# Kernel optimization log

Hardware: AMD Instinct MI355X
Metric: run time of the kernel (lower is better)

The kernel has to match this reference:

```python
import jax, jax.numpy as jnp
import numpy as np

D_MODEL, N_HEADS, RANK = 1024, 16, 32
HEAD_DIM = D_MODEL // N_HEADS
B, S = 4, 2048


def setup_inputs() -> dict:
    key = jax.random.key(0)
    ks = jax.random.split(key, 8)
    inp = {
        "x": jax.random.normal(ks[0], (B, S, D_MODEL), dtype=jnp.float32),
        "mask": jnp.ones((B, S), dtype=jnp.int32),
        "qkv_u": jax.random.normal(ks[1], (D_MODEL, RANK), jnp.float32) / D_MODEL ** 0.5,
        "qkv_v": jax.random.normal(ks[2], (RANK, 3 * D_MODEL), jnp.float32) / RANK ** 0.5,
        "qkv_b": jnp.zeros((3 * D_MODEL,), jnp.float32),
        "u_attn": jax.random.normal(ks[3], (N_HEADS, HEAD_DIM, RANK), jnp.float32) / HEAD_DIM ** 0.5,
        "v_attn": jax.random.normal(ks[4], (N_HEADS, RANK, HEAD_DIM), jnp.float32) / RANK ** 0.5,
        "out_u": jax.random.normal(ks[5], (D_MODEL, RANK), jnp.float32) / D_MODEL ** 0.5,
        "out_v": jax.random.normal(ks[6], (RANK, D_MODEL), jnp.float32) / RANK ** 0.5,
        "out_b": jnp.zeros((D_MODEL,), jnp.float32),
    }
    return inp


def reference(x, mask, qkv_u, qkv_v, qkv_b, u_attn, v_attn, out_u, out_v, out_b):
    bs, seq_len, d_model = x.shape
    n_heads, head_dim, rank = u_attn.shape
    scale = 1.0 / jnp.sqrt(jnp.float32(rank))

    # Low-rank QKV projection: [B,S,3D]
    qkv = (x @ qkv_u) @ qkv_v + qkv_b
    q, k, v = jnp.split(qkv, 3, axis=-1)

    def to_heads(t):  # [B,S,D] -> [B,H,S,hd]
        return t.reshape(bs, seq_len, n_heads, head_dim).transpose(0, 2, 1, 3)

    q, k, v = to_heads(q), to_heads(k), to_heads(v)

    # Rank-projected Q/K: [B,H,S,r]
    q_low = jnp.einsum("bhsd,hdr->bhsr", q, u_attn)
    k_low = jnp.einsum("bhtd,hdr->bhtr", k, u_attn)
    scores = jnp.einsum("bhsr,bhtr->bhst", q_low, k_low) * scale

    # mask: [B,S] keys; masked_fill where mask == 0
    scores = jnp.where(mask[:, None, None, :] == 0, jnp.float32(-jnp.inf), scores)
    attn = jax.nn.softmax(scores, axis=-1)  # dropout is identity in eval

    v_low = jnp.einsum("bhtd,hdr->bhtr", v, u_attn)
    context_low = jnp.einsum("bhst,bhtr->bhsr", attn, v_low)
    context = jnp.einsum("bhsr,hrd->bhsd", context_low, v_attn)
    context = context.transpose(0, 2, 1, 3).reshape(bs, seq_len, d_model)

    return (context @ out_u) @ out_v + out_b
```

## Files before the change

### kernel.cpp

```cpp
#include <hip/hip_runtime.h>
#include <hip/hip_bf16.h>

typedef unsigned int u32;
typedef unsigned short u16;
typedef __attribute__((ext_vector_type(8))) __bf16 bf16x8;
typedef __attribute__((ext_vector_type(16))) float f32x16;
typedef __attribute__((ext_vector_type(2))) unsigned int u32x2;

#define QSCALE 0.25505418f
#define MFMA __builtin_amdgcn_mfma_f32_32x32x16_bf16

static __device__ __forceinline__ u16 f2b(float f) {
  __hip_bfloat16 h = __float2bfloat16(f);
  return *reinterpret_cast<u16*>(&h);
}
static __device__ __forceinline__ u32 cvtpk(float lo, float hi) {
  u32 r;
  asm("v_cvt_pk_bf16_f32 %0, %1, %2" : "=v"(r) : "v"(lo), "v"(hi));
  return r;
}

static __device__ __forceinline__ float xhalf_sum(float v) {
#if __has_builtin(__builtin_amdgcn_permlane32_swap)
  u32 a = __float_as_uint(v);
  u32x2 r = __builtin_amdgcn_permlane32_swap(a, a, false, false);
  return __uint_as_float(r[0]) + __uint_as_float(r[1]);
#else
  return v + __shfl_xor(v, 32);
#endif
}

static __device__ __forceinline__ int tau(int p) {
  int g = p >> 2;
  int gk = (g & 4) | ((g & 1) << 1) | ((g >> 1) & 1);
  return (gk << 2) | (p & 3);
}

__global__ __launch_bounds__(256) void k_prep(const float* __restrict__ qkv_v,
                                              const float* __restrict__ qkv_b,
                                              const float* __restrict__ u_attn,
                                              const float* __restrict__ v_attn,
                                              const float* __restrict__ out_u,
                                              const float* __restrict__ qkv_u,
                                              const float* __restrict__ out_v,
                                              u16* __restrict__ WQT, u16* __restrict__ WKT,
                                              u16* __restrict__ WVT, float* __restrict__ BQKV,
                                              u16* __restrict__ WOT, u16* __restrict__ UT,
                                              u16* __restrict__ OVT) {
  int blk = blockIdx.x;
  int tid = threadIdx.x;
  if (blk < 16) {
    int h = blk;
    int r = tid & 31, g = tid >> 5;
    for (int rp = g; rp < 32; rp += 8) {
      float aq = 0.f, ak = 0.f, av = 0.f;
      for (int d = 0; d < 64; ++d) {
        float u = u_attn[(h * 64 + d) * 32 + r];
        aq += qkv_v[rp * 3072 + h * 64 + d] * u;
        ak += qkv_v[rp * 3072 + 1024 + h * 64 + d] * u;
        av += qkv_v[rp * 3072 + 2048 + h * 64 + d] * u;
      }
      WQT[(h * 32 + r) * 32 + rp] = f2b(aq);
      WKT[(h * 32 + r) * 32 + rp] = f2b(ak);
      WVT[(h * 32 + r) * 32 + rp] = f2b(av);
    }
    for (int rr = g; rr < 32; rr += 8) {
      float a = 0.f;
      for (int d = 0; d < 64; ++d)
        a += v_attn[(h * 32 + rr) * 64 + d] * out_u[(h * 64 + d) * 32 + r];
      WOT[r * 512 + h * 32 + rr] = f2b(a);
    }
    if (tid < 32) {
      float aq = 0.f, ak = 0.f, av = 0.f;
      for (int d = 0; d < 64; ++d) {
        float u = u_attn[(h * 64 + d) * 32 + r];
        aq += qkv_b[h * 64 + d] * u;
        ak += qkv_b[1024 + h * 64 + d] * u;
        av += qkv_b[2048 + h * 64 + d] * u;
      }
      BQKV[h * 32 + r] = aq;
      BQKV[512 + h * 32 + r] = ak;
      BQKV[1024 + h * 32 + r] = av;
    }
  } else if (blk < 24) {
    int kb = (blk - 16) * 128;
    for (int i = tid; i < 4096; i += 256) {
      int r = i >> 7, kl = i & 127;
      UT[r * 1024 + kb + kl] = f2b(qkv_u[(kb + kl) * 32 + r]);
    }
  } else {
    int db = (blk - 24) * 128;
    for (int i = tid; i < 4096; i += 256) {
      int dl = i >> 5, r = i & 31;
      OVT[(db + dl) * 32 + r] = f2b(out_v[r * 1024 + db + dl]);
    }
  }
}

__global__ __launch_bounds__(256) void k_proj(const float* __restrict__ x,
                                              const u16* __restrict__ UT,
                                              u16* __restrict__ T) {
  __shared__ float red[4][32][33];
  int tid = threadIdx.x;
  int w = tid >> 6, l = tid & 63, lo = l & 31, hi = l >> 5;
  int m0 = blockIdx.x * 32;
  const float* xp = x + (size_t)(m0 + lo) * 1024 + w * 256 + hi * 8;
  const u16* up = UT + lo * 1024 + w * 256 + hi * 8;
  f32x16 acc = {};
  for (int s = 0; s < 16; ++s) {
    float4 x0 = *(const float4*)(xp);
    float4 x1 = *(const float4*)(xp + 4);
    xp += 16;
    union { bf16x8 v; u32 u[4]; } af;
    af.u[0] = cvtpk(x0.x, x0.y);
    af.u[1] = cvtpk(x0.z, x0.w);
    af.u[2] = cvtpk(x1.x, x1.y);
    af.u[3] = cvtpk(x1.z, x1.w);
    bf16x8 bf = *(const bf16x8*)(up);
    up += 16;
    acc = MFMA(af.v, bf, acc, 0, 0, 0);
  }
#pragma unroll
  for (int i = 0; i < 16; ++i)
    red[w][(i & 3) + 8 * (i >> 2) + 4 * hi][lo] = acc[i];
  __syncthreads();
  int m = tid >> 3, c = (tid & 7) * 4;
  float v0 = red[0][m][c + 0] + red[1][m][c + 0] + red[2][m][c + 0] + red[3][m][c + 0];
  float v1 = red[0][m][c + 1] + red[1][m][c + 1] + red[2][m][c + 1] + red[3][m][c + 1];
  float v2 = red[0][m][c + 2] + red[1][m][c + 2] + red[2][m][c + 2] + red[3][m][c + 2];
  float v3 = red[0][m][c + 3] + red[1][m][c + 3] + red[2][m][c + 3] + red[3][m][c + 3];
  uint2 o;
  o.x = cvtpk(v0, v1);
  o.y = cvtpk(v2, v3);
  *(uint2*)(T + (size_t)(m0 + m) * 32 + c) = o;
}

__global__ __launch_bounds__(256) void k_lowproj(const u16* __restrict__ T,
                                                 const u16* __restrict__ WQT,
                                                 const u16* __restrict__ WKT,
                                                 const u16* __restrict__ WVT,
                                                 const float* __restrict__ BQKV,
                                                 u16* __restrict__ QL, u16* __restrict__ KF,
                                                 u16* __restrict__ VF) {
  __shared__ float vtf[32][132];
  int tid = threadIdx.x;
  int w = tid >> 6, l = tid & 63, lo = l & 31, hi = l >> 5;
  int blk = blockIdx.x;
  int bh = blk >> 4, sb = (blk & 15) * 128;
  int b = bh >> 4, h = bh & 15;
  int s0 = sb + w * 32;

  const u16* wq = WQT + (h * 32 + lo) * 32 + hi * 8;
  const u16* wk = WKT + (h * 32 + lo) * 32 + hi * 8;
  const u16* wv = WVT + (h * 32 + lo) * 32 + hi * 8;
  bf16x8 aq0 = *(const bf16x8*)(wq), aq1 = *(const bf16x8*)(wq + 16);
  bf16x8 ak0 = *(const bf16x8*)(wk), ak1 = *(const bf16x8*)(wk + 16);
  bf16x8 av0 = *(const bf16x8*)(wv), av1 = *(const bf16x8*)(wv + 16);

  const u16* tp = T + (size_t)(b * 2048 + s0 + lo) * 32 + hi * 8;
  bf16x8 tb0 = *(const bf16x8*)(tp), tb1 = *(const bf16x8*)(tp + 16);

  f32x16 cq = {}, ck = {}, cv = {};
  cq = MFMA(aq0, tb0, cq, 0, 0, 0);
  cq = MFMA(aq1, tb1, cq, 0, 0, 0);
  ck = MFMA(ak0, tb0, ck, 0, 0, 0);
  ck = MFMA(ak1, tb1, ck, 0, 0, 0);
  cv = MFMA(av0, tb0, cv, 0, 0, 0);
  cv = MFMA(av1, tb1, cv, 0, 0, 0);

  size_t sg = (size_t)bh * 2048 + s0 + lo;
  size_t tbase = (size_t)bh * 65536 + (size_t)((sb >> 5) + w) * 1024;
  int slp = w * 32 + tau(lo);
#pragma unroll
  for (int g2 = 0; g2 < 4; ++g2) {
    float4 bq4 = *(const float4*)(BQKV + h * 32 + g2 * 8 + 4 * hi);
    float4 bk4 = *(const float4*)(BQKV + 512 + h * 32 + g2 * 8 + 4 * hi);
    float4 bv4 = *(const float4*)(BQKV + 1024 + h * 32 + g2 * 8 + 4 * hi);
    float q0 = (cq[4 * g2 + 0] + bq4.x) * QSCALE;
    float q1 = (cq[4 * g2 + 1] + bq4.y) * QSCALE;
    float q2 = (cq[4 * g2 + 2] + bq4.z) * QSCALE;
    float q3 = (cq[4 * g2 + 3] + bq4.w) * QSCALE;
    uint2 qo; qo.x = cvtpk(q0, q1); qo.y = cvtpk(q2, q3);
    *(uint2*)(QL + sg * 32 + g2 * 8 + 4 * hi) = qo;
    uint2 ko;
    ko.x = cvtpk(ck[4 * g2 + 0] + bk4.x, ck[4 * g2 + 1] + bk4.y);
    ko.y = cvtpk(ck[4 * g2 + 2] + bk4.z, ck[4 * g2 + 3] + bk4.w);
    *(uint2*)(KF + tbase + (g2 >> 1) * 512 + (g2 & 1) * 256 + lo * 8 + 4 * hi) = ko;
    int rbase = g2 * 8 + 4 * hi;
    vtf[rbase + 0][slp] = cv[4 * g2 + 0] + bv4.x;
    vtf[rbase + 1][slp] = cv[4 * g2 + 1] + bv4.y;
    vtf[rbase + 2][slp] = cv[4 * g2 + 2] + bv4.z;
    vtf[rbase + 3][slp] = cv[4 * g2 + 3] + bv4.w;
  }
  __syncthreads();
  for (int u = tid; u < 512; u += 256) {
    int r = u >> 4, su = (u & 15) * 8;
    const float* src = &vtf[r][su];
    uint4 o;
    o.x = cvtpk(src[0], src[1]);
    o.y = cvtpk(src[2], src[3]);
    o.z = cvtpk(src[4], src[5]);
    o.w = cvtpk(src[6], src[7]);
    int c = su & 31, tloc = su >> 5;
    *(uint4*)(VF + (size_t)bh * 65536 + (size_t)((sb >> 5) + tloc) * 1024 +
              (c >> 4) * 512 + ((c >> 3) & 1) * 256 + r * 8) = o;
  }
}

__global__ __launch_bounds__(256) void k_attn(const u16* __restrict__ QL,
                                              const u16* __restrict__ KF,
                                              const u16* __restrict__ VF,
                                              const int* __restrict__ mask,
                                              u16* __restrict__ CTX) {
  __shared__ float pacc[2][64][17];
  __shared__ float pl[2][64];
  __shared__ u32 cls[64][17];
  int tid = threadIdx.x;
  int wave = tid >> 6, l = tid & 63, lo = l & 31, hi = l >> 5;
  int blk = blockIdx.x;
  int xcd = blk & 7, slot = blk >> 3;
  int bh = xcd * 8 + (slot >> 5);
  int qpair = slot & 31;
  int qi = wave & 1;
  int khalf = wave >> 1;
  int qt = qpair * 2 + qi;
  int b = bh >> 4, h = bh & 15;

  const int* mk = mask + b * 2048;

  int q = qt * 32 + lo;
  const u16* qp = QL + (size_t)bh * 65536 + q * 32 + hi * 8;
  bf16x8 qb0 = *(const bf16x8*)(qp);
  bf16x8 qb1 = *(const bf16x8*)(qp + 16);

  size_t fbase = (size_t)bh * 65536 + (size_t)khalf * 32768 + l * 8;
  const u16* kp = KF + fbase;
  const u16* vp = VF + fbase;

  f32x16 acc = {};
  float l_run = 0.f;

  int mall = 1;
  for (int i = l; i < 2048; i += 64) mall &= (mk[i] != 0) ? 1 : 0;

  if (__all(mall)) {
#pragma unroll 1
    for (int kt = 0; kt < 32; ++kt) {
      bf16x8 ka0 = *(const bf16x8*)(kp);
      bf16x8 ka1 = *(const bf16x8*)(kp + 512);
      kp += 1024;
      f32x16 sc = {};
      sc = MFMA(ka0, qb0, sc, 0, 0, 0);
      sc = MFMA(ka1, qb1, sc, 0, 0, 0);
      bf16x8 va0 = *(const bf16x8*)(vp);
      bf16x8 va1 = *(const bf16x8*)(vp + 512);
      vp += 1024;
      union { bf16x8 v; u32 u[4]; } fa;
      float a0 = __builtin_amdgcn_exp2f(sc[0]);
      float a1 = __builtin_amdgcn_exp2f(sc[1]);
      float a2 = __builtin_amdgcn_exp2f(sc[2]);
      float a3 = __builtin_amdgcn_exp2f(sc[3]);
      fa.u[0] = cvtpk(a0, a1);
      fa.u[1] = cvtpk(a2, a3);
      float t0 = (a0 + a1) + (a2 + a3);
      a0 = __builtin_amdgcn_exp2f(sc[4]);
      a1 = __builtin_amdgcn_exp2f(sc[5]);
      a2 = __builtin_amdgcn_exp2f(sc[6]);
      a3 = __builtin_amdgcn_exp2f(sc[7]);
      fa.u[2] = cvtpk(a0, a1);
      fa.u[3] = cvtpk(a2, a3);
      float t1 = (a0 + a1) + (a2 + a3);
      acc = MFMA(va0, fa.v, acc, 0, 0, 0);
      union { bf16x8 v; u32 u[4]; } fc;
      a0 = __builtin_amdgcn_exp2f(sc[8]);
      a1 = __builtin_amdgcn_exp2f(sc[9]);
      a2 = __builtin_amdgcn_exp2f(sc[10]);
      a3 = __builtin_amdgcn_exp2f(sc[11]);
      fc.u[0] = cvtpk(a0, a1);
      fc.u[1] = cvtpk(a2, a3);
      float t2 = (a0 + a1) + (a2 + a3);
      a0 = __builtin_amdgcn_exp2f(sc[12]);
      a1 = __builtin_amdgcn_exp2f(sc[13]);
      a2 = __builtin_amdgcn_exp2f(sc[14]);
      a3 = __builtin_amdgcn_exp2f(sc[15]);
      fc.u[2] = cvtpk(a0, a1);
      fc.u[3] = cvtpk(a2, a3);
      float t3 = (a0 + a1) + (a2 + a3);
      acc = MFMA(va1, fc.v, acc, 0, 0, 0);
      l_run += (t0 + t1) + (t2 + t3);
    }
  } else {
    const int* mp = mk + khalf * 1024 + lo;
#pragma unroll 1
    for (int kt = 0; kt < 32; ++kt) {
      unsigned long long bm = __ballot(mp[0] != 0);
      mp += 32;
      bf16x8 ka0 = *(const bf16x8*)(kp);
      bf16x8 ka1 = *(const bf16x8*)(kp + 512);
      kp += 1024;
      f32x16 sc = {};
      sc = MFMA(ka0, qb0, sc, 0, 0, 0);
      sc = MFMA(ka1, qb1, sc, 0, 0, 0);
      u32 km = (u32)bm;
#pragma unroll
      for (int i = 0; i < 16; ++i) {
        int key = (i & 3) + 8 * (i >> 2) + 4 * hi;
        if (!((km >> key) & 1)) sc[i] = -3.0e38f;
      }
      bf16x8 va0 = *(const bf16x8*)(vp);
      bf16x8 va1 = *(const bf16x8*)(vp + 512);
      vp += 1024;
      union { bf16x8 v; u32 u[4]; } fa;
      float a0 = __builtin_amdgcn_exp2f(sc[0]);
      float a1 = __builtin_amdgcn_exp2f(sc[1]);
      float a2 = __builtin_amdgcn_exp2f(sc[2]);
      float a3 = __builtin_amdgcn_exp2f(sc[3]);
      fa.u[0] = cvtpk(a0, a1);
      fa.u[1] = cvtpk(a2, a3);
      float t0 = (a0 + a1) + (a2 + a3);
      a0 = __builtin_amdgcn_exp2f(sc[4]);
      a1 = __builtin_amdgcn_exp2f(sc[5]);
      a2 = __builtin_amdgcn_exp2f(sc[6]);
      a3 = __builtin_amdgcn_exp2f(sc[7]);
      fa.u[2] = cvtpk(a0, a1);
      fa.u[3] = cvtpk(a2, a3);
      float t1 = (a0 + a1) + (a2 + a3);
      acc = MFMA(va0, fa.v, acc, 0, 0, 0);
      union { bf16x8 v; u32 u[4]; } fc;
      a0 = __builtin_amdgcn_exp2f(sc[8]);
      a1 = __builtin_amdgcn_exp2f(sc[9]);
      a2 = __builtin_amdgcn_exp2f(sc[10]);
      a3 = __builtin_amdgcn_exp2f(sc[11]);
      fc.u[0] = cvtpk(a0, a1);
      fc.u[1] = cvtpk(a2, a3);
      float t2 = (a0 + a1) + (a2 + a3);
      a0 = __builtin_amdgcn_exp2f(sc[12]);
      a1 = __builtin_amdgcn_exp2f(sc[13]);
      a2 = __builtin_amdgcn_exp2f(sc[14]);
      a3 = __builtin_amdgcn_exp2f(sc[15]);
      fc.u[2] = cvtpk(a0, a1);
      fc.u[3] = cvtpk(a2, a3);
      float t3 = (a0 + a1) + (a2 + a3);
      acc = MFMA(va1, fc.v, acc, 0, 0, 0);
      l_run += (t0 + t1) + (t2 + t3);
    }
  }

  if (khalf) {
#pragma unroll
    for (int i = 0; i < 16; ++i) pacc[qi][l][i] = acc[i];
    pl[qi][l] = l_run;
  }
  __syncthreads();
  if (!khalf) {
#pragma unroll
    for (int i = 0; i < 16; ++i) acc[i] += pacc[qi][l][i];
    l_run += pl[qi][l];
    l_run = xhalf_sum(l_run);
    float inv = 1.0f / l_run;
    int qloc = qi * 32 + lo;
#pragma unroll
    for (int g2 = 0; g2 < 4; ++g2) {
      cls[qloc][g2 * 4 + 2 * hi] = cvtpk(acc[4 * g2 + 0] * inv, acc[4 * g2 + 1] * inv);
      cls[qloc][g2 * 4 + 2 * hi + 1] = cvtpk(acc[4 * g2 + 2] * inv, acc[4 * g2 + 3] * inv);
    }
  }
  __syncthreads();
  int s_loc = tid >> 2, quad = tid & 3;
  int srow = qpair * 64 + s_loc;
  const u32* src = &cls[s_loc][quad * 4];
  uint4 v0;
  v0.x = src[0]; v0.y = src[1]; v0.z = src[2]; v0.w = src[3];
  u16* dst = CTX + (((size_t)(b * 2048 + srow)) * 16 + h) * 32 + quad * 8;
  *(uint4*)(dst) = v0;
}

__global__ __launch_bounds__(256) void k_epi1(const u16* __restrict__ CTX,
                                              const u16* __restrict__ WOT,
                                              u16* __restrict__ YL) {
  __shared__ float red[4][32][33];
  int tid = threadIdx.x;
  int w = tid >> 6, l = tid & 63, lo = l & 31, hi = l >> 5;
  int s0 = blockIdx.x * 32;
  const u16* cp = CTX + (size_t)(s0 + lo) * 512 + w * 128 + hi * 8;
  const u16* wp = WOT + lo * 512 + w * 128 + hi * 8;
  f32x16 acc = {};
  for (int st = 0; st < 8; ++st) {
    bf16x8 a = *(const bf16x8*)(cp);
    bf16x8 bb = *(const bf16x8*)(wp);
    cp += 16;
    wp += 16;
    acc = MFMA(a, bb, acc, 0, 0, 0);
  }
#pragma unroll
  for (int i = 0; i < 16; ++i)
    red[w][(i & 3) + 8 * (i >> 2) + 4 * hi][lo] = acc[i];
  __syncthreads();
  int m = tid >> 3, c = (tid & 7) * 4;
  float v0 = red[0][m][c + 0] + red[1][m][c + 0] + red[2][m][c + 0] + red[3][m][c + 0];
  float v1 = red[0][m][c + 1] + red[1][m][c + 1] + red[2][m][c + 1] + red[3][m][c + 1];
  float v2 = red[0][m][c + 2] + red[1][m][c + 2] + red[2][m][c + 2] + red[3][m][c + 2];
  float v3 = red[0][m][c + 3] + red[1][m][c + 3] + red[2][m][c + 3] + red[3][m][c + 3];
  uint2 o;
  o.x = cvtpk(v0, v1);
  o.y = cvtpk(v2, v3);
  *(uint2*)(YL + (size_t)(s0 + m) * 32 + c) = o;
}

__global__ __launch_bounds__(256) void k_epi2(const u16* __restrict__ YL,
                                              const u16* __restrict__ OVT,
                                              const float* __restrict__ out_b,
                                              float* __restrict__ out) {
  __shared__ float ol[32][133];
  int tid = threadIdx.x;
  int w = tid >> 6, l = tid & 63, lo = l & 31, hi = l >> 5;
  int blk = blockIdx.x;
  int s0 = (blk >> 3) * 32;
  int d0 = (blk & 7) * 128;
  int dw = d0 + w * 32;
  const u16* ap = OVT + (size_t)(dw + lo) * 32 + hi * 8;
  bf16x8 a0 = *(const bf16x8*)(ap), a1 = *(const bf16x8*)(ap + 16);
  const u16* bp = YL + (size_t)(s0 + lo) * 32 + hi * 8;
  bf16x8 b0 = *(const bf16x8*)(bp), b1 = *(const bf16x8*)(bp + 16);
  f32x16 acc = {};
  acc = MFMA(a0, b0, acc, 0, 0, 0);
  acc = MFMA(a1, b1, acc, 0, 0, 0);
#pragma unroll
  for (int i = 0; i < 16; ++i)
    ol[lo][w * 32 + (i & 3) + 8 * (i >> 2) + 4 * hi] = acc[i];
  __syncthreads();
  for (int u = tid; u < 1024; u += 256) {
    int s = u >> 5, c = (u & 31) * 4;
    float4 ob = *(const float4*)(out_b + d0 + c);
    float4 o;
    o.x = ol[s][c + 0] + ob.x;
    o.y = ol[s][c + 1] + ob.y;
    o.z = ol[s][c + 2] + ob.z;
    o.w = ol[s][c + 3] + ob.w;
    *(float4*)(out + (size_t)(s0 + s) * 1024 + d0 + c) = o;
  }
}

extern "C" void kernel_launch(void* const* d_in, const int* in_sizes, int n_in,
                              void* d_out, int out_size, void* d_ws, size_t ws_size,
                              hipStream_t stream) {
  const float* x = (const float*)d_in[0];
  const int* mask = (const int*)d_in[1];
  const float* qkv_u = (const float*)d_in[2];
  const float* qkv_v = (const float*)d_in[3];
  const float* qkv_b = (const float*)d_in[4];
  const float* u_attn = (const float*)d_in[5];
  const float* v_attn = (const float*)d_in[6];
  const float* out_u = (const float*)d_in[7];
  const float* out_v = (const float*)d_in[8];
  const float* out_b = (const float*)d_in[9];
  float* out = (float*)d_out;

  char* w = (char*)d_ws;
  u16* WQT = (u16*)(w + 0);
  u16* WKT = (u16*)(w + (32 << 10));
  u16* WVT = (u16*)(w + (64 << 10));
  float* BQ = (float*)(w + (96 << 10));
  u16* WOT = (u16*)(w + (104 << 10));
  u16* UT = (u16*)(w + (136 << 10));
  u16* OVT = (u16*)(w + (200 << 10));
  u16* T = (u16*)(w + (1 << 20));
  u16* QL = (u16*)(w + (2 << 20));
  u16* KF = (u16*)(w + (10 << 20));
  u16* VF = (u16*)(w + (18 << 20));
  u16* CTX = (u16*)(w + (26 << 20));
  u16* YL = (u16*)(w + (34 << 20));

  k_prep<<<32, 256, 0, stream>>>(qkv_v, qkv_b, u_attn, v_attn, out_u, qkv_u, out_v,
                                 WQT, WKT, WVT, BQ, WOT, UT, OVT);
  k_proj<<<256, 256, 0, stream>>>(x, UT, T);
  k_lowproj<<<1024, 256, 0, stream>>>(T, WQT, WKT, WVT, BQ, QL, KF, VF);
  k_attn<<<2048, 256, 0, stream>>>(QL, KF, VF, mask, CTX);
  k_epi1<<<256, 256, 0, stream>>>(CTX, WOT, YL);
  k_epi2<<<2048, 256, 0, stream>>>(YL, OVT, out_b, out);
}
```

Measured before the change: 132.3 us.

## Fuse output projection epilogues into one kernel and raise MFMA priority in attention

Merges the two output-projection kernels into one: the low-rank intermediate is kept in shared memory and each block loops over all output column tiles, removing a launch and the global round trip of the intermediate. It also wraps the attention MFMAs with s_setprio so matrix instructions are favored over the interleaved exp work. The fused epilogue runs only 256 blocks that each write a full row slab of the output, which reduces parallelism for the large output store.

```diff
diff --git a/kernel.cpp b/kernel.cpp
--- a/kernel.cpp
+++ b/kernel.cpp
@@ -250,8 +250,10 @@
       bf16x8 ka1 = *(const bf16x8*)(kp + 512);
       kp += 1024;
       f32x16 sc = {};
+      __builtin_amdgcn_s_setprio(1);
       sc = MFMA(ka0, qb0, sc, 0, 0, 0);
       sc = MFMA(ka1, qb1, sc, 0, 0, 0);
+      __builtin_amdgcn_s_setprio(0);
       bf16x8 va0 = *(const bf16x8*)(vp);
       bf16x8 va1 = *(const bf16x8*)(vp + 512);
       vp += 1024;
@@ -270,7 +272,9 @@
       fa.u[2] = cvtpk(a0, a1);
       fa.u[3] = cvtpk(a2, a3);
       float t1 = (a0 + a1) + (a2 + a3);
+      __builtin_amdgcn_s_setprio(1);
       acc = MFMA(va0, fa.v, acc, 0, 0, 0);
+      __builtin_amdgcn_s_setprio(0);
       union { bf16x8 v; u32 u[4]; } fc;
       a0 = __builtin_amdgcn_exp2f(sc[8]);
       a1 = __builtin_amdgcn_exp2f(sc[9]);
@@ -286,7 +290,9 @@
       fc.u[2] = cvtpk(a0, a1);
       fc.u[3] = cvtpk(a2, a3);
       float t3 = (a0 + a1) + (a2 + a3);
+      __builtin_amdgcn_s_setprio(1);
       acc = MFMA(va1, fc.v, acc, 0, 0, 0);
+      __builtin_amdgcn_s_setprio(0);
       l_run += (t0 + t1) + (t2 + t3);
     }
   } else {
@@ -375,10 +381,14 @@
   *(uint4*)(dst) = v0;
 }
 
-__global__ __launch_bounds__(256) void k_epi1(const u16* __restrict__ CTX,
-                                              const u16* __restrict__ WOT,
-                                              u16* __restrict__ YL) {
+__global__ __launch_bounds__(256) void k_epi(const u16* __restrict__ CTX,
+                                             const u16* __restrict__ WOT,
+                                             const u16* __restrict__ OVT,
+                                             const float* __restrict__ out_b,
+                                             float* __restrict__ out) {
   __shared__ float red[4][32][33];
+  __shared__ u32 yl[32][17];
+  __shared__ float ol[32][133];
   int tid = threadIdx.x;
   int w = tid >> 6, l = tid & 63, lo = l & 31, hi = l >> 5;
   int s0 = blockIdx.x * 32;
@@ -396,48 +406,45 @@
   for (int i = 0; i < 16; ++i)
     red[w][(i & 3) + 8 * (i >> 2) + 4 * hi][lo] = acc[i];
   __syncthreads();
-  int m = tid >> 3, c = (tid & 7) * 4;
-  float v0 = red[0][m][c + 0] + red[1][m][c + 0] + red[2][m][c + 0] + red[3][m][c + 0];
-  float v1 = red[0][m][c + 1] + red[1][m][c + 1] + red[2][m][c + 1] + red[3][m][c + 1];
-  float v2 = red[0][m][c + 2] + red[1][m][c + 2] + red[2][m][c + 2] + red[3][m][c + 2];
-  float v3 = red[0][m][c + 3] + red[1][m][c + 3] + red[2][m][c + 3] + red[3][m][c + 3];
-  uint2 o;
-  o.x = cvtpk(v0, v1);
-  o.y = cvtpk(v2, v3);
-  *(uint2*)(YL + (size_t)(s0 + m) * 32 + c) = o;
-}
-
-__global__ __launch_bounds__(256) void k_epi2(const u16* __restrict__ YL,
-                                              const u16* __restrict__ OVT,
-                                              const float* __restrict__ out_b,
-                                              float* __restrict__ out) {
-  __shared__ float ol[32][133];
-  int tid = threadIdx.x;
-  int w = tid >> 6, l = tid & 63, lo = l & 31, hi = l >> 5;
-  int blk = blockIdx.x;
-  int s0 = (blk >> 3) * 32;
-  int d0 = (blk & 7) * 128;
-  int dw = d0 + w * 32;
-  const u16* ap = OVT + (size_t)(dw + lo) * 32 + hi * 8;
-  bf16x8 a0 = *(const bf16x8*)(ap), a1 = *(const bf16x8*)(ap + 16);
-  const u16* bp = YL + (size_t)(s0 + lo) * 32 + hi * 8;
-  bf16x8 b0 = *(const bf16x8*)(bp), b1 = *(const bf16x8*)(bp + 16);
-  f32x16 acc = {};
-  acc = MFMA(a0, b0, acc, 0, 0, 0);
-  acc = MFMA(a1, b1, acc, 0, 0, 0);
-#pragma unroll
-  for (int i = 0; i < 16; ++i)
-    ol[lo][w * 32 + (i & 3) + 8 * (i >> 2) + 4 * hi] = acc[i];
-  __syncthreads();
-  for (int u = tid; u < 1024; u += 256) {
-    int s = u >> 5, c = (u & 31) * 4;
-    float4 ob = *(const float4*)(out_b + d0 + c);
-    float4 o;
-    o.x = ol[s][c + 0] + ob.x;
-    o.y = ol[s][c + 1] + ob.y;
-    o.z = ol[s][c + 2] + ob.z;
-    o.w = ol[s][c + 3] + ob.w;
-    *(float4*)(out + (size_t)(s0 + s) * 1024 + d0 + c) = o;
+  {
+    int m = tid >> 3, c = (tid & 7) * 4;
+    float v0 = red[0][m][c + 0] + red[1][m][c + 0] + red[2][m][c + 0] + red[3][m][c + 0];
+    float v1 = red[0][m][c + 1] + red[1][m][c + 1] + red[2][m][c + 1] + red[3][m][c + 1];
+    float v2 = red[0][m][c + 2] + red[1][m][c + 2] + red[2][m][c + 2] + red[3][m][c + 2];
+    float v3 = red[0][m][c + 3] + red[1][m][c + 3] + red[2][m][c + 3] + red[3][m][c + 3];
+    yl[m][(c >> 1) + 0] = cvtpk(v0, v1);
+    yl[m][(c >> 1) + 1] = cvtpk(v2, v3);
+  }
+  __syncthreads();
+  union { bf16x8 v; u32 u[4]; } ub0, ub1;
+#pragma unroll
+  for (int j = 0; j < 4; ++j) {
+    ub0.u[j] = yl[lo][hi * 4 + j];
+    ub1.u[j] = yl[lo][8 + hi * 4 + j];
+  }
+  for (int dt = 0; dt < 8; ++dt) {
+    int d0 = dt * 128;
+    int dw = d0 + w * 32;
+    const u16* ap = OVT + (size_t)(dw + lo) * 32 + hi * 8;
+    bf16x8 a0 = *(const bf16x8*)(ap), a1 = *(const bf16x8*)(ap + 16);
+    f32x16 a2 = {};
+    a2 = MFMA(a0, ub0.v, a2, 0, 0, 0);
+    a2 = MFMA(a1, ub1.v, a2, 0, 0, 0);
+#pragma unroll
+    for (int i = 0; i < 16; ++i)
+      ol[lo][w * 32 + (i & 3) + 8 * (i >> 2) + 4 * hi] = a2[i];
+    __syncthreads();
+    for (int u = tid; u < 1024; u += 256) {
+      int s = u >> 5, c = (u & 31) * 4;
+      float4 ob = *(const float4*)(out_b + d0 + c);
+      float4 o;
+      o.x = ol[s][c + 0] + ob.x;
+      o.y = ol[s][c + 1] + ob.y;
+      o.z = ol[s][c + 2] + ob.z;
+      o.w = ol[s][c + 3] + ob.w;
+      *(float4*)(out + (size_t)(s0 + s) * 1024 + d0 + c) = o;
+    }
+    __syncthreads();
   }
 }
 
@@ -469,13 +476,11 @@
   u16* KF = (u16*)(w + (10 << 20));
   u16* VF = (u16*)(w + (18 << 20));
   u16* CTX = (u16*)(w + (26 << 20));
-  u16* YL = (u16*)(w + (34 << 20));
 
   k_prep<<<32, 256, 0, stream>>>(qkv_v, qkv_b, u_attn, v_attn, out_u, qkv_u, out_v,
                                  WQT, WKT, WVT, BQ, WOT, UT, OVT);
   k_proj<<<256, 256, 0, stream>>>(x, UT, T);
   k_lowproj<<<1024, 256, 0, stream>>>(T, WQT, WKT, WVT, BQ, QL, KF, VF);
   k_attn<<<2048, 256, 0, stream>>>(QL, KF, VF, mask, CTX);
-  k_epi1<<<256, 256, 0, stream>>>(CTX, WOT, YL);
-  k_epi2<<<2048, 256, 0, stream>>>(YL, OVT, out_b, out);
-}
+  k_epi<<<256, 256, 0, stream>>>(CTX, WOT, OVT, out_b, out);
+}
```

Result: slower. 137.8 us (+4.2%).
